# Performance work log

Measured on AMD Instinct MI355X. Metric: run time of the kernel, lower is better.

## Reference

```python
import jax, jax.numpy as jnp
import numpy as np

B, S, H = 2, 2048, 2048
NH = 16
HD = H // NH
SCALE = 1.0 / float(np.sqrt(HD))


def setup_inputs() -> dict:
    key = jax.random.key(0)
    ks = jax.random.split(key, 4)
    x = jax.random.normal(ks[0], (B, S, H), dtype=jnp.float32)
    # causal mask: 1 = attend, 0 = masked (masked_fill where mask == 0)
    attn_mask = jnp.tril(jnp.ones((S, S), dtype=jnp.int32))[None, None, :, :]
    w_qkv = jax.random.normal(ks[1], (3 * H, H), dtype=jnp.float32) * (1.0 / np.sqrt(H))
    b_qkv = jnp.zeros((3 * H,), dtype=jnp.float32)
    w_out = jax.random.normal(ks[2], (H, H), dtype=jnp.float32) * (1.0 / np.sqrt(H))
    b_out = jnp.zeros((H,), dtype=jnp.float32)
    return {"x": x, "attn_mask": attn_mask, "w_qkv": w_qkv, "b_qkv": b_qkv,
            "w_out": w_out, "b_out": b_out}


def reference(x, attn_mask, w_qkv, b_qkv, w_out, b_out):
    bsz, seq_len, hidden = x.shape
    # qkv projection (torch Linear: x @ W.T + b); TP gather is identity on 1 device
    qkv = jnp.einsum('bsh,oh->bso', x, w_qkv) + b_qkv  # [B,S,3H]
    q, k, v = jnp.split(qkv, 3, axis=-1)
    def shape(t):  # [B,S,H] -> [B,NH,S,HD]
        return t.reshape(bsz, seq_len, NH, HD).transpose(0, 2, 1, 3)
    q, k, v = shape(q), shape(k), shape(v)
    attn = jnp.einsum('bhqd,bhkd->bhqk', q, k) * SCALE  # [B,NH,S,S]
    attn = jnp.where(attn_mask == 0, jnp.float32(-10000.0), attn)
    attn = jax.nn.softmax(attn, axis=-1)  # dropout_p = 0 -> identity
    ctx = jnp.einsum('bhqk,bhkd->bhqd', attn, v)
    ctx = ctx.transpose(0, 2, 1, 3).reshape(bsz, seq_len, hidden)
    out = jnp.einsum('bsh,oh->bso', ctx, w_out) + b_out
    return out
```

## Files before the change

### kernel.cpp

```cpp
#include <hip/hip_runtime.h>
#include <hip/hip_bf16.h>
#include <stdint.h>

#define B_ 2
#define S_ 2048
#define H_ 2048
#define NH_ 16
#define HD_ 128
#define SCALE_ 0.08838834764831845f
#define QSCALE_ 0.12751743558230564f

typedef __attribute__((ext_vector_type(8))) short bf16x8;
typedef __attribute__((ext_vector_type(4))) float f32x4;

__device__ __forceinline__ unsigned short f2bf(float f) {
  union { float f; unsigned int u; } c;
  c.f = f;
  unsigned int u = c.u;
  unsigned int r = (u + 0x7fffu + ((u >> 16) & 1u)) >> 16;
  return (unsigned short)r;
}

__device__ __forceinline__ unsigned int cvt_pk_bf16(float lo, float hi) {
  unsigned int r;
  asm("v_cvt_pk_bf16_f32 %0, %1, %2" : "=v"(r) : "v"(lo), "v"(hi));
  return r;
}

__global__ void cvt_f32_bf16_k(const float* __restrict__ in,
                               unsigned short* __restrict__ out, int n4) {
  int i = blockIdx.x * blockDim.x + threadIdx.x;
  if (i < n4) {
    float4 v = reinterpret_cast<const float4*>(in)[i];
    ushort4 o;
    o.x = f2bf(v.x); o.y = f2bf(v.y); o.z = f2bf(v.z); o.w = f2bf(v.w);
    reinterpret_cast<ushort4*>(out)[i] = o;
  }
}

template <int MODE>
__global__ __launch_bounds__(256) void gemm_bt_k(
    const unsigned short* __restrict__ A,
    const unsigned short* __restrict__ Bm,
    const float* __restrict__ bias,
    int K, int N,
    float* __restrict__ outf,
    unsigned short* __restrict__ Qp,
    unsigned short* __restrict__ Kp,
    unsigned short* __restrict__ Vn) {
  __shared__ unsigned short Al[128 * 32];
  __shared__ unsigned short Bl[128 * 32];
  const int tid = threadIdx.x;
  const int lane = tid & 63;
  const int w = tid >> 6;
  const int wr = w >> 1, wc = w & 1;
  const int brow = blockIdx.y * 128, bcol = blockIdx.x * 128;
  const int lr = lane & 15, lg = lane >> 4;
  f32x4 acc[4][4] = {};

  for (int kb = 0; kb < K; kb += 32) {
    __syncthreads();
#pragma unroll
    for (int p = 0; p < 2; ++p) {
      int c = p * 256 + tid;
      int row = c >> 2, kc = (c & 3) * 8;
      __builtin_amdgcn_global_load_lds(
          (const __attribute__((address_space(1))) unsigned int*)(A + (size_t)(brow + row) * K + kb + kc),
          (__attribute__((address_space(3))) unsigned int*)(Al + c * 8), 16, 0, 0);
      __builtin_amdgcn_global_load_lds(
          (const __attribute__((address_space(1))) unsigned int*)(Bm + (size_t)(bcol + row) * K + kb + kc),
          (__attribute__((address_space(3))) unsigned int*)(Bl + c * 8), 16, 0, 0);
    }
    __syncthreads();
    bf16x8 af[4], bfr[4];
#pragma unroll
    for (int m = 0; m < 4; ++m)
      af[m] = *reinterpret_cast<const bf16x8*>(&Al[(wr * 64 + m * 16 + lr) * 32 + lg * 8]);
#pragma unroll
    for (int n = 0; n < 4; ++n)
      bfr[n] = *reinterpret_cast<const bf16x8*>(&Bl[(wc * 64 + n * 16 + lr) * 32 + lg * 8]);
#pragma unroll
    for (int m = 0; m < 4; ++m)
#pragma unroll
      for (int n = 0; n < 4; ++n)
        acc[m][n] = __builtin_amdgcn_mfma_f32_16x16x32_bf16(af[m], bfr[n], acc[m][n], 0, 0, 0);
  }

#pragma unroll
  for (int m = 0; m < 4; ++m) {
#pragma unroll
    for (int n = 0; n < 4; ++n) {
      int gcol = bcol + wc * 64 + n * 16 + lr;
      int grow0 = brow + wr * 64 + m * 16 + lg * 4;
      float bv = bias[gcol];
      if (MODE == 1) {
#pragma unroll
        for (int r = 0; r < 4; ++r)
          outf[(size_t)(grow0 + r) * N + gcol] = acc[m][n][r] + bv;
      } else {
        int region = gcol >> 11;
        int o = gcol & 2047;
        int head = o >> 7, d = o & 127;
#pragma unroll
        for (int r = 0; r < 4; ++r) {
          int grow = grow0 + r;
          int b = grow >> 11, s = grow & 2047;
          float fv = acc[m][n][r] + bv;
          if (region == 0)
            Qp[((size_t)(b * NH_ + head) * S_ + s) * HD_ + d] = f2bf(fv * QSCALE_);
          else if (region == 1)
            Kp[((size_t)(b * NH_ + head) * S_ + s) * HD_ + d] = f2bf(fv);
          else
            Vn[(size_t)grow * H_ + o] = f2bf(fv);
        }
      }
    }
  }
}

__global__ void transpose_v_k(const unsigned short* __restrict__ Vn,
                              unsigned short* __restrict__ Vt) {
  __shared__ unsigned short t[32][33];
  int bh = blockIdx.z;
  int b = bh >> 4, h = bh & 15;
  int s0 = blockIdx.x * 32, d0 = blockIdx.y * 32;
  int x = threadIdx.x, y0 = threadIdx.y;
#pragma unroll
  for (int yy = 0; yy < 32; yy += 8) {
    int s = s0 + y0 + yy;
    t[y0 + yy][x] = Vn[((size_t)(b * S_ + s)) * H_ + h * HD_ + d0 + x];
  }
  __syncthreads();
#pragma unroll
  for (int yy = 0; yy < 32; yy += 8) {
    int d = d0 + y0 + yy;
    Vt[((size_t)(bh * HD_ + d)) * S_ + s0 + x] = t[x][y0 + yy];
  }
}

__global__ __launch_bounds__(512, 4) void flash_attn_k(
    const unsigned short* __restrict__ Qp,
    const unsigned short* __restrict__ Kp,
    const unsigned short* __restrict__ Vt,
    unsigned short* __restrict__ ctx) {
  __shared__ unsigned short Kl[64 * 128];
  __shared__ unsigned short Vl[128 * 64];
  __shared__ unsigned short Pl[8][16 * 72];

  const int tid = threadIdx.x;
  const int lane = tid & 63, w = tid >> 6;
  const int lr = lane & 15, lg = lane >> 4;
  const int bid = blockIdx.x;
  const int bh = bid & 31;
  const int qi = 15 - (bid >> 5);
  const int b = bh >> 4, h = bh & 15;
  const int qtile = qi * 128;
  const int qbase = qtile + w * 16;

  const unsigned short* Qh = Qp + (size_t)bh * S_ * HD_;
  const unsigned short* Kh = Kp + (size_t)bh * S_ * HD_;
  const unsigned short* Vh = Vt + (size_t)bh * HD_ * S_;

  bf16x8 qf[4];
#pragma unroll
  for (int dc = 0; dc < 4; ++dc)
    qf[dc] = *reinterpret_cast<const bf16x8*>(Qh + (size_t)(qbase + lr) * HD_ + dc * 32 + lg * 8);

  f32x4 acc_o[8] = {};
  float m_r = -1e30f, l_r = 0.f;

  const int nkb = 2 * qi + 2;
  for (int kb = 0; kb < nkb; ++kb) {
    __syncthreads();
    const unsigned short* Kbase = Kh + (size_t)(kb * 64) * HD_;
    const unsigned short* Vbase = Vh + kb * 64;
#pragma unroll
    for (int c2 = 0; c2 < 2; ++c2) {
      int chunk = c2 * 512 + tid;
      int krow = chunk >> 4;
      int kcol = (chunk & 15) << 4;
      int kswz = kcol ^ ((krow & 7) << 4);
      __builtin_amdgcn_global_load_lds(
          (const __attribute__((address_space(1))) unsigned int*)(Kbase + krow * HD_ + (kswz >> 1)),
          (__attribute__((address_space(3))) unsigned int*)(Kl + chunk * 8), 16, 0, 0);
      int vrow = chunk >> 3;
      int vcol = (chunk & 7) << 4;
      int vswz = vcol ^ ((vrow & 7) << 4);
      __builtin_amdgcn_global_load_lds(
          (const __attribute__((address_space(1))) unsigned int*)(Vbase + (size_t)vrow * S_ + (vswz >> 1)),
          (__attribute__((address_space(3))) unsigned int*)(Vl + chunk * 8), 16, 0, 0);
    }
    __syncthreads();

    const bool live = (kb * 64 <= qbase + 15);
    if (live) {
      f32x4 sa[4] = {};
#pragma unroll
      for (int n = 0; n < 4; ++n) {
        int row = n * 16 + lr;
#pragma unroll
        for (int dc = 0; dc < 4; ++dc) {
          int byte = row * 256 + dc * 64 + lg * 16;
          byte ^= (row & 7) << 4;
          bf16x8 kf = *reinterpret_cast<const bf16x8*>(
              reinterpret_cast<const char*>(Kl) + byte);
          sa[n] = __builtin_amdgcn_mfma_f32_16x16x32_bf16(kf, qf[dc], sa[n], 0, 0, 0);
        }
      }

      if (kb * 64 + 63 > qbase) {
        int rowq = qbase + lr;
#pragma unroll
        for (int n = 0; n < 4; ++n) {
          int col0 = kb * 64 + n * 16 + lg * 4;
#pragma unroll
          for (int r = 0; r < 4; ++r)
            if (col0 + r > rowq) sa[n][r] = -1e30f;
        }
      }

      float mx4[4];
#pragma unroll
      for (int n = 0; n < 4; ++n)
        mx4[n] = fmaxf(fmaxf(sa[n][0], sa[n][1]), fmaxf(sa[n][2], sa[n][3]));
      float mx = fmaxf(fmaxf(mx4[0], mx4[1]), fmaxf(mx4[2], mx4[3]));
      mx = fmaxf(mx, __shfl_xor(mx, 16));
      mx = fmaxf(mx, __shfl_xor(mx, 32));
      float mnew = fmaxf(m_r, mx);
      float alpha = exp2f(m_r - mnew);

      float p[4][4];
      float rsn[4];
#pragma unroll
      for (int n = 0; n < 4; ++n) {
#pragma unroll
        for (int r = 0; r < 4; ++r)
          p[n][r] = exp2f(sa[n][r] - mnew);
        rsn[n] = (p[n][0] + p[n][1]) + (p[n][2] + p[n][3]);
      }
      float rs = (rsn[0] + rsn[1]) + (rsn[2] + rsn[3]);
      rs += __shfl_xor(rs, 16);
      rs += __shfl_xor(rs, 32);
      l_r = l_r * alpha + rs;
      m_r = mnew;

#pragma unroll
      for (int n = 0; n < 4; ++n) {
        uint2 pk;
        pk.x = cvt_pk_bf16(p[n][0], p[n][1]);
        pk.y = cvt_pk_bf16(p[n][2], p[n][3]);
        *reinterpret_cast<uint2*>(&Pl[w][lr * 72 + n * 16 + lg * 4]) = pk;
      }

      float al[4];
#pragma unroll
      for (int r = 0; r < 4; ++r)
        al[r] = __shfl(alpha, lg * 4 + r);
#pragma unroll
      for (int nc = 0; nc < 8; ++nc)
#pragma unroll
        for (int r = 0; r < 4; ++r)
          acc_o[nc][r] *= al[r];

      bf16x8 pa[2];
#pragma unroll
      for (int ks = 0; ks < 2; ++ks)
        pa[ks] = *reinterpret_cast<const bf16x8*>(&Pl[w][lr * 72 + ks * 32 + lg * 8]);
#pragma unroll
      for (int nc = 0; nc < 8; ++nc) {
        int row = nc * 16 + lr;
#pragma unroll
        for (int ks = 0; ks < 2; ++ks) {
          int byte = row * 128 + ks * 64 + lg * 16;
          byte ^= (row & 7) << 4;
          bf16x8 vf = *reinterpret_cast<const bf16x8*>(
              reinterpret_cast<const char*>(Vl) + byte);
          acc_o[nc] = __builtin_amdgcn_mfma_f32_16x16x32_bf16(pa[ks], vf, acc_o[nc], 0, 0, 0);
        }
      }
    }
  }

  float linv = 1.f / l_r;
  float li[4];
#pragma unroll
  for (int r = 0; r < 4; ++r)
    li[r] = __shfl(linv, lg * 4 + r);
#pragma unroll
  for (int nc = 0; nc < 8; ++nc) {
#pragma unroll
    for (int r = 0; r < 4; ++r) {
      int s = qbase + lg * 4 + r;
      ctx[((size_t)(b * S_ + s)) * H_ + h * HD_ + nc * 16 + lr] = f2bf(acc_o[nc][r] * li[r]);
    }
  }
}

extern "C" void kernel_launch(void* const* d_in, const int* in_sizes, int n_in,
                              void* d_out, int out_size, void* d_ws, size_t ws_size,
                              hipStream_t stream) {
  const float* x = (const float*)d_in[0];
  const float* w_qkv = (const float*)d_in[2];
  const float* b_qkv = (const float*)d_in[3];
  const float* w_out = (const float*)d_in[4];
  const float* b_out = (const float*)d_in[5];
  float* out = (float*)d_out;

  char* ws = (char*)d_ws;
  unsigned short* xb    = (unsigned short*)(ws);
  unsigned short* wqkvb = (unsigned short*)(ws + 16777216);
  unsigned short* woutb = (unsigned short*)(ws + 41943040);
  unsigned short* Qp    = (unsigned short*)(ws + 50331648);
  unsigned short* Kp    = (unsigned short*)(ws + 67108864);
  unsigned short* Vn    = (unsigned short*)(ws + 83886080);
  unsigned short* Vt    = (unsigned short*)(ws + 100663296);
  unsigned short* ctx   = (unsigned short*)(ws + 117440512);

  hipLaunchKernelGGL(cvt_f32_bf16_k, dim3(8192), dim3(256), 0, stream, x, xb, 2097152);
  hipLaunchKernelGGL(cvt_f32_bf16_k, dim3(12288), dim3(256), 0, stream, w_qkv, wqkvb, 3145728);
  hipLaunchKernelGGL(cvt_f32_bf16_k, dim3(4096), dim3(256), 0, stream, w_out, woutb, 1048576);

  hipLaunchKernelGGL((gemm_bt_k<0>), dim3(48, 32), dim3(256), 0, stream,
                     xb, wqkvb, b_qkv, 2048, 6144, (float*)nullptr, Qp, Kp, Vn);

  hipLaunchKernelGGL(transpose_v_k, dim3(64, 4, 32), dim3(32, 8), 0, stream, Vn, Vt);

  hipLaunchKernelGGL(flash_attn_k, dim3(512), dim3(512), 0, stream, Qp, Kp, Vt, ctx);

  hipLaunchKernelGGL((gemm_bt_k<1>), dim3(16, 32), dim3(256), 0, stream,
                     ctx, woutb, b_out, 2048, 2048, out,
                     (unsigned short*)nullptr, (unsigned short*)nullptr, (unsigned short*)nullptr);
}
```

Measured before the change: 457.8 us.

## Replace GEMM with 256x256-tile, double-buffered, 8-wave ping-pong MFMA kernel

Replaces the single-buffered 128x128 GEMM used for the QKV and output projections with a 512-thread kernel. It computes 256x256 tiles and stages 64-wide K slices into a 128 KB double-buffered, XOR-swizzled LDS region using global_load_lds. The main loop interleaves async prefetch of future K slices with MFMA phases, using explicit vmcnt/lgkmcnt waits, barriers and s_setprio. This is meant to hide global-load latency and raise MFMA utilisation. In exchange, the large tiles give fewer blocks (384 for QKV, 128 for the output projection), which risks load imbalance and idle CUs.

```diff
diff --git a/kernel.cpp b/kernel.cpp
--- a/kernel.cpp
+++ b/kernel.cpp
@@ -12,6 +12,9 @@
 
 typedef __attribute__((ext_vector_type(8))) short bf16x8;
 typedef __attribute__((ext_vector_type(4))) float f32x4;
+
+#define AS1 __attribute__((address_space(1)))
+#define AS3 __attribute__((address_space(3)))
 
 __device__ __forceinline__ unsigned short f2bf(float f) {
   union { float f; unsigned int u; } c;
@@ -39,7 +42,7 @@
 }
 
 template <int MODE>
-__global__ __launch_bounds__(256) void gemm_bt_k(
+__global__ __launch_bounds__(512, 2) void gemm8_k(
     const unsigned short* __restrict__ A,
     const unsigned short* __restrict__ Bm,
     const float* __restrict__ bias,
@@ -48,50 +51,135 @@
     unsigned short* __restrict__ Qp,
     unsigned short* __restrict__ Kp,
     unsigned short* __restrict__ Vn) {
-  __shared__ unsigned short Al[128 * 32];
-  __shared__ unsigned short Bl[128 * 32];
+  extern __shared__ char smem[];
   const int tid = threadIdx.x;
-  const int lane = tid & 63;
-  const int w = tid >> 6;
-  const int wr = w >> 1, wc = w & 1;
-  const int brow = blockIdx.y * 128, bcol = blockIdx.x * 128;
+  const int lane = tid & 63, w = tid >> 6;
+  const int wr = w >> 2, wc = w & 3;
   const int lr = lane & 15, lg = lane >> 4;
-  f32x4 acc[4][4] = {};
-
-  for (int kb = 0; kb < K; kb += 32) {
-    __syncthreads();
-#pragma unroll
-    for (int p = 0; p < 2; ++p) {
-      int c = p * 256 + tid;
-      int row = c >> 2, kc = (c & 3) * 8;
+  const int brow = blockIdx.y * 256, bcol = blockIdx.x * 256;
+  const int NT = K >> 6;
+
+  f32x4 acc[8][4] = {};
+
+  auto stageA = [&](int u, int kh) {
+#pragma unroll
+    for (int j = 0; j < 2; ++j) {
+      int chunk = j * 512 + tid;
+      int row = chunk >> 2;
+      int colb = (chunk & 3) << 4;
+      int scol = colb ^ ((row & 3) << 4);
       __builtin_amdgcn_global_load_lds(
-          (const __attribute__((address_space(1))) unsigned int*)(A + (size_t)(brow + row) * K + kb + kc),
-          (__attribute__((address_space(3))) unsigned int*)(Al + c * 8), 16, 0, 0);
+          (const AS1 unsigned int*)(A + (size_t)(brow + row) * K + u * 64 + kh * 32 + (scol >> 1)),
+          (AS3 unsigned int*)(smem + ((u & 1) * 2 + kh) * 16384 + chunk * 16), 16, 0, 0);
+    }
+  };
+  auto stageB = [&](int u, int kh) {
+#pragma unroll
+    for (int j = 0; j < 2; ++j) {
+      int chunk = j * 512 + tid;
+      int row = chunk >> 2;
+      int colb = (chunk & 3) << 4;
+      int scol = colb ^ ((row & 3) << 4);
       __builtin_amdgcn_global_load_lds(
-          (const __attribute__((address_space(1))) unsigned int*)(Bm + (size_t)(bcol + row) * K + kb + kc),
-          (__attribute__((address_space(3))) unsigned int*)(Bl + c * 8), 16, 0, 0);
-    }
-    __syncthreads();
-    bf16x8 af[4], bfr[4];
-#pragma unroll
-    for (int m = 0; m < 4; ++m)
-      af[m] = *reinterpret_cast<const bf16x8*>(&Al[(wr * 64 + m * 16 + lr) * 32 + lg * 8]);
-#pragma unroll
-    for (int n = 0; n < 4; ++n)
-      bfr[n] = *reinterpret_cast<const bf16x8*>(&Bl[(wc * 64 + n * 16 + lr) * 32 + lg * 8]);
-#pragma unroll
-    for (int m = 0; m < 4; ++m)
-#pragma unroll
-      for (int n = 0; n < 4; ++n)
-        acc[m][n] = __builtin_amdgcn_mfma_f32_16x16x32_bf16(af[m], bfr[n], acc[m][n], 0, 0, 0);
-  }
-
-#pragma unroll
-  for (int m = 0; m < 4; ++m) {
+          (const AS1 unsigned int*)(Bm + (size_t)(bcol + row) * K + u * 64 + kh * 32 + (scol >> 1)),
+          (AS3 unsigned int*)(smem + 65536 + ((u & 1) * 2 + kh) * 16384 + chunk * 16), 16, 0, 0);
+    }
+  };
+  auto ldA = [&](int d, int kh, int m) -> bf16x8 {
+    int row = wr * 128 + m * 16 + lr;
+    int byte = (d * 2 + kh) * 16384 + row * 64 + ((lg * 16) ^ ((row & 3) << 4));
+    return *reinterpret_cast<const bf16x8*>(smem + byte);
+  };
+  auto ldB = [&](int d, int kh, int n) -> bf16x8 {
+    int row = wc * 64 + n * 16 + lr;
+    int byte = 65536 + (d * 2 + kh) * 16384 + row * 64 + ((lg * 16) ^ ((row & 3) << 4));
+    return *reinterpret_cast<const bf16x8*>(smem + byte);
+  };
+
+  stageA(0, 0); stageB(0, 0); stageA(0, 1); stageB(0, 1);
+  stageA(1, 0); stageB(1, 0); stageA(1, 1);
+  asm volatile("s_waitcnt vmcnt(6)" ::: "memory");
+  __builtin_amdgcn_s_barrier();
+
+  for (int T = 0; T < NT; ++T) {
+    const int d = T & 1;
+    bf16x8 af[8], b0, b1;
+
+#pragma unroll
+    for (int m = 0; m < 8; ++m) af[m] = ldA(d, 0, m);
+    b0 = ldB(d, 0, 0); b1 = ldB(d, 0, 1);
+    if (T + 1 < NT) stageB(T + 1, 1);
+    __builtin_amdgcn_sched_barrier(0);
+    __builtin_amdgcn_s_barrier();
+    asm volatile("s_waitcnt lgkmcnt(0)" ::: "memory");
+    __builtin_amdgcn_sched_barrier(0);
+    __builtin_amdgcn_s_setprio(1);
+#pragma unroll
+    for (int m = 0; m < 8; ++m) {
+      acc[m][0] = __builtin_amdgcn_mfma_f32_16x16x32_bf16(af[m], b0, acc[m][0], 0, 0, 0);
+      acc[m][1] = __builtin_amdgcn_mfma_f32_16x16x32_bf16(af[m], b1, acc[m][1], 0, 0, 0);
+    }
+    __builtin_amdgcn_s_setprio(0);
+    __builtin_amdgcn_s_barrier();
+
+    b0 = ldB(d, 0, 2); b1 = ldB(d, 0, 3);
+    if (T + 2 < NT) stageA(T + 2, 0);
+    __builtin_amdgcn_sched_barrier(0);
+    __builtin_amdgcn_s_barrier();
+    asm volatile("s_waitcnt lgkmcnt(0)" ::: "memory");
+    __builtin_amdgcn_sched_barrier(0);
+    __builtin_amdgcn_s_setprio(1);
+#pragma unroll
+    for (int m = 0; m < 8; ++m) {
+      acc[m][2] = __builtin_amdgcn_mfma_f32_16x16x32_bf16(af[m], b0, acc[m][2], 0, 0, 0);
+      acc[m][3] = __builtin_amdgcn_mfma_f32_16x16x32_bf16(af[m], b1, acc[m][3], 0, 0, 0);
+    }
+    __builtin_amdgcn_s_setprio(0);
+    __builtin_amdgcn_s_barrier();
+
+#pragma unroll
+    for (int m = 0; m < 8; ++m) af[m] = ldA(d, 1, m);
+    b0 = ldB(d, 1, 0); b1 = ldB(d, 1, 1);
+    if (T + 2 < NT) stageB(T + 2, 0);
+    __builtin_amdgcn_sched_barrier(0);
+    __builtin_amdgcn_s_barrier();
+    asm volatile("s_waitcnt lgkmcnt(0)" ::: "memory");
+    __builtin_amdgcn_sched_barrier(0);
+    __builtin_amdgcn_s_setprio(1);
+#pragma unroll
+    for (int m = 0; m < 8; ++m) {
+      acc[m][0] = __builtin_amdgcn_mfma_f32_16x16x32_bf16(af[m], b0, acc[m][0], 0, 0, 0);
+      acc[m][1] = __builtin_amdgcn_mfma_f32_16x16x32_bf16(af[m], b1, acc[m][1], 0, 0, 0);
+    }
+    __builtin_amdgcn_s_setprio(0);
+    __builtin_amdgcn_s_barrier();
+
+    b0 = ldB(d, 1, 2); b1 = ldB(d, 1, 3);
+    if (T + 2 < NT) stageA(T + 2, 1);
+    __builtin_amdgcn_sched_barrier(0);
+    __builtin_amdgcn_s_barrier();
+    asm volatile("s_waitcnt lgkmcnt(0)" ::: "memory");
+    __builtin_amdgcn_sched_barrier(0);
+    __builtin_amdgcn_s_setprio(1);
+#pragma unroll
+    for (int m = 0; m < 8; ++m) {
+      acc[m][2] = __builtin_amdgcn_mfma_f32_16x16x32_bf16(af[m], b0, acc[m][2], 0, 0, 0);
+      acc[m][3] = __builtin_amdgcn_mfma_f32_16x16x32_bf16(af[m], b1, acc[m][3], 0, 0, 0);
+    }
+    __builtin_amdgcn_s_setprio(0);
+    if (T + 2 < NT)
+      asm volatile("s_waitcnt vmcnt(6)" ::: "memory");
+    else if (T + 1 < NT)
+      asm volatile("s_waitcnt vmcnt(0)" ::: "memory");
+    __builtin_amdgcn_s_barrier();
+  }
+
+#pragma unroll
+  for (int m = 0; m < 8; ++m) {
 #pragma unroll
     for (int n = 0; n < 4; ++n) {
       int gcol = bcol + wc * 64 + n * 16 + lr;
-      int grow0 = brow + wr * 64 + m * 16 + lg * 4;
+      int grow0 = brow + wr * 128 + m * 16 + lg * 4;
       float bv = bias[gcol];
       if (MODE == 1) {
 #pragma unroll
@@ -100,16 +188,16 @@
       } else {
         int region = gcol >> 11;
         int o = gcol & 2047;
-        int head = o >> 7, d = o & 127;
+        int head = o >> 7, dd = o & 127;
 #pragma unroll
         for (int r = 0; r < 4; ++r) {
           int grow = grow0 + r;
           int b = grow >> 11, s = grow & 2047;
           float fv = acc[m][n][r] + bv;
           if (region == 0)
-            Qp[((size_t)(b * NH_ + head) * S_ + s) * HD_ + d] = f2bf(fv * QSCALE_);
+            Qp[((size_t)(b * NH_ + head) * S_ + s) * HD_ + dd] = f2bf(fv * QSCALE_);
           else if (region == 1)
-            Kp[((size_t)(b * NH_ + head) * S_ + s) * HD_ + d] = f2bf(fv);
+            Kp[((size_t)(b * NH_ + head) * S_ + s) * HD_ + dd] = f2bf(fv);
           else
             Vn[(size_t)grow * H_ + o] = f2bf(fv);
         }
@@ -181,14 +269,14 @@
       int kcol = (chunk & 15) << 4;
       int kswz = kcol ^ ((krow & 7) << 4);
       __builtin_amdgcn_global_load_lds(
-          (const __attribute__((address_space(1))) unsigned int*)(Kbase + krow * HD_ + (kswz >> 1)),
-          (__attribute__((address_space(3))) unsigned int*)(Kl + chunk * 8), 16, 0, 0);
+          (const AS1 unsigned int*)(Kbase + krow * HD_ + (kswz >> 1)),
+          (AS3 unsigned int*)(Kl + chunk * 8), 16, 0, 0);
       int vrow = chunk >> 3;
       int vcol = (chunk & 7) << 4;
       int vswz = vcol ^ ((vrow & 7) << 4);
       __builtin_amdgcn_global_load_lds(
-          (const __attribute__((address_space(1))) unsigned int*)(Vbase + (size_t)vrow * S_ + (vswz >> 1)),
-          (__attribute__((address_space(3))) unsigned int*)(Vl + chunk * 8), 16, 0, 0);
+          (const AS1 unsigned int*)(Vbase + (size_t)vrow * S_ + (vswz >> 1)),
+          (AS3 unsigned int*)(Vl + chunk * 8), 16, 0, 0);
     }
     __syncthreads();
 
@@ -316,18 +404,23 @@
   unsigned short* Vt    = (unsigned short*)(ws + 100663296);
   unsigned short* ctx   = (unsigned short*)(ws + 117440512);
 
+  hipFuncSetAttribute(reinterpret_cast<const void*>(gemm8_k<0>),
+                      hipFuncAttributeMaxDynamicSharedMemorySize, 131072);
+  hipFuncSetAttribute(reinterpret_cast<const void*>(gemm8_k<1>),
+                      hipFuncAttributeMaxDynamicSharedMemorySize, 131072);
+
   hipLaunchKernelGGL(cvt_f32_bf16_k, dim3(8192), dim3(256), 0, stream, x, xb, 2097152);
   hipLaunchKernelGGL(cvt_f32_bf16_k, dim3(12288), dim3(256), 0, stream, w_qkv, wqkvb, 3145728);
   hipLaunchKernelGGL(cvt_f32_bf16_k, dim3(4096), dim3(256), 0, stream, w_out, woutb, 1048576);
 
-  hipLaunchKernelGGL((gemm_bt_k<0>), dim3(48, 32), dim3(256), 0, stream,
+  hipLaunchKernelGGL((gemm8_k<0>), dim3(24, 16), dim3(512), 131072, stream,
                      xb, wqkvb, b_qkv, 2048, 6144, (float*)nullptr, Qp, Kp, Vn);
 
   hipLaunchKernelGGL(transpose_v_k, dim3(64, 4, 32), dim3(32, 8), 0, stream, Vn, Vt);
 
   hipLaunchKernelGGL(flash_attn_k, dim3(512), dim3(512), 0, stream, Qp, Kp, Vt, ctx);
 
-  hipLaunchKernelGGL((gemm_bt_k<1>), dim3(16, 32), dim3(256), 0, stream,
+  hipLaunchKernelGGL((gemm8_k<1>), dim3(8, 16), dim3(512), 131072, stream,
                      ctx, woutb, b_out, 2048, 2048, out,
                      (unsigned short*)nullptr, (unsigned short*)nullptr, (unsigned short*)nullptr);
 }
```

Measured after the change: 468.7 us. 2.4% more time.

## Replace QKV projection GEMM with 256x256 double-buffered pipelined MFMA kernel

Applied to the files above, without the earlier changes.

Swaps the QKV projection GEMM for a new kernel using 256x256 block tiles, 512 threads, 64-wide K steps and double-buffered LDS (128 KB dynamic shared memory) with swizzled layout. Loads for the next K tile are interleaved between MFMA phases, with barriers and priority hints around them. The larger tile increases data reuse and hides global load latency. The cost is heavy LDS use and register pressure, and only 384 blocks on the device, which lowers occupancy. The output projection stays on the old 128x128 kernel.

```diff
diff --git a/kernel.cpp b/kernel.cpp
--- a/kernel.cpp
+++ b/kernel.cpp
@@ -7,11 +7,13 @@
 #define H_ 2048
 #define NH_ 16
 #define HD_ 128
-#define SCALE_ 0.08838834764831845f
 #define QSCALE_ 0.12751743558230564f
 
 typedef __attribute__((ext_vector_type(8))) short bf16x8;
 typedef __attribute__((ext_vector_type(4))) float f32x4;
+
+#define AS1 __attribute__((address_space(1)))
+#define AS3 __attribute__((address_space(3)))
 
 __device__ __forceinline__ unsigned short f2bf(float f) {
   union { float f; unsigned int u; } c;
@@ -38,16 +40,169 @@
   }
 }
 
-template <int MODE>
-__global__ __launch_bounds__(256) void gemm_bt_k(
+__global__ __launch_bounds__(512, 2) void gemm256_k(
     const unsigned short* __restrict__ A,
     const unsigned short* __restrict__ Bm,
     const float* __restrict__ bias,
     int K, int N,
-    float* __restrict__ outf,
     unsigned short* __restrict__ Qp,
     unsigned short* __restrict__ Kp,
     unsigned short* __restrict__ Vn) {
+  extern __shared__ char smem[];
+  const int tid = threadIdx.x;
+  const int lane = tid & 63, w = tid >> 6;
+  const int wr = w >> 2, wc = w & 3;
+  const int lr = lane & 15, lg = lane >> 4;
+  const int brow = blockIdx.y * 256, bcol = blockIdx.x * 256;
+  const int NT = K >> 6;
+
+  f32x4 acc[8][4] = {};
+
+  auto stage = [&](const unsigned short* __restrict__ src, int ldsbase,
+                   int gr0, int kc0) {
+#pragma unroll
+    for (int j = 0; j < 2; ++j) {
+      int chunk = j * 512 + tid;
+      int row = chunk >> 3;
+      int colb = (chunk & 7) << 4;
+      int scol = colb ^ (((row >> 2) & 1) << 5);
+      __builtin_amdgcn_global_load_lds(
+          (const AS1 unsigned int*)(src + (size_t)(gr0 + row) * K + kc0 + (scol >> 1)),
+          (AS3 unsigned int*)(smem + ldsbase + chunk * 16), 16, 0, 0);
+    }
+  };
+  auto aoff = [&](int d, int h) { return (d * 2 + h) * 16384; };
+  auto boff = [&](int d, int h) { return 65536 + (d * 2 + h) * 16384; };
+
+  auto ldA = [&](int d, int m, int kk) -> bf16x8 {
+    int rowr = m * 16 + lr;
+    int off = (kk * 64 + lg * 16) ^ (((rowr >> 2) & 1) << 5);
+    return *reinterpret_cast<const bf16x8*>(smem + aoff(d, wr) + rowr * 128 + off);
+  };
+  auto ldB = [&](int d, int n, int kk) -> bf16x8 {
+    int row = wc * 64 + n * 16 + lr;
+    int h = row >> 7, rowr = row & 127;
+    int off = (kk * 64 + lg * 16) ^ (((rowr >> 2) & 1) << 5);
+    return *reinterpret_cast<const bf16x8*>(smem + boff(d, h) + rowr * 128 + off);
+  };
+
+  stage(A,  aoff(0, 0), brow +   0, 0);
+  stage(A,  aoff(0, 1), brow + 128, 0);
+  stage(Bm, boff(0, 0), bcol +   0, 0);
+  stage(Bm, boff(0, 1), bcol + 128, 0);
+  stage(Bm, boff(1, 0), bcol +   0, 64);
+  stage(Bm, boff(1, 1), bcol + 128, 64);
+  asm volatile("s_waitcnt vmcnt(4)" ::: "memory");
+  __builtin_amdgcn_s_barrier();
+
+  for (int T = 0; T < NT; ++T) {
+    const int d = T & 1;
+    bf16x8 af[4][2], bA[2][2], bB[2][2];
+
+#pragma unroll
+    for (int m = 0; m < 4; ++m) { af[m][0] = ldA(d, m, 0); af[m][1] = ldA(d, m, 1); }
+    bA[0][0] = ldB(d, 0, 0); bA[0][1] = ldB(d, 0, 1);
+    bA[1][0] = ldB(d, 1, 0); bA[1][1] = ldB(d, 1, 1);
+    if (T + 1 < NT) stage(A, aoff(d ^ 1, 0), brow + 0, (T + 1) * 64);
+    __builtin_amdgcn_s_barrier();
+    asm volatile("s_waitcnt lgkmcnt(0)" ::: "memory");
+    __builtin_amdgcn_sched_barrier(0);
+    __builtin_amdgcn_s_setprio(1);
+#pragma unroll
+    for (int m = 0; m < 4; ++m)
+#pragma unroll
+      for (int n = 0; n < 2; ++n) {
+        acc[m][n] = __builtin_amdgcn_mfma_f32_16x16x32_bf16(af[m][0], bA[n][0], acc[m][n], 0, 0, 0);
+        acc[m][n] = __builtin_amdgcn_mfma_f32_16x16x32_bf16(af[m][1], bA[n][1], acc[m][n], 0, 0, 0);
+      }
+    __builtin_amdgcn_s_setprio(0);
+    __builtin_amdgcn_s_barrier();
+
+    bB[0][0] = ldB(d, 2, 0); bB[0][1] = ldB(d, 2, 1);
+    bB[1][0] = ldB(d, 3, 0); bB[1][1] = ldB(d, 3, 1);
+    if (T + 1 < NT) stage(A, aoff(d ^ 1, 1), brow + 128, (T + 1) * 64);
+    __builtin_amdgcn_s_barrier();
+    asm volatile("s_waitcnt lgkmcnt(0)" ::: "memory");
+    __builtin_amdgcn_sched_barrier(0);
+    __builtin_amdgcn_s_setprio(1);
+#pragma unroll
+    for (int m = 0; m < 4; ++m)
+#pragma unroll
+      for (int n = 0; n < 2; ++n) {
+        acc[m][n + 2] = __builtin_amdgcn_mfma_f32_16x16x32_bf16(af[m][0], bB[n][0], acc[m][n + 2], 0, 0, 0);
+        acc[m][n + 2] = __builtin_amdgcn_mfma_f32_16x16x32_bf16(af[m][1], bB[n][1], acc[m][n + 2], 0, 0, 0);
+      }
+    __builtin_amdgcn_s_setprio(0);
+    __builtin_amdgcn_s_barrier();
+
+#pragma unroll
+    for (int m = 0; m < 4; ++m) { af[m][0] = ldA(d, m + 4, 0); af[m][1] = ldA(d, m + 4, 1); }
+    if (T + 2 < NT) stage(Bm, boff(d, 0), bcol + 0, (T + 2) * 64);
+    __builtin_amdgcn_s_barrier();
+    asm volatile("s_waitcnt lgkmcnt(0)" ::: "memory");
+    __builtin_amdgcn_sched_barrier(0);
+    __builtin_amdgcn_s_setprio(1);
+#pragma unroll
+    for (int m = 0; m < 4; ++m)
+#pragma unroll
+      for (int n = 0; n < 2; ++n) {
+        acc[m + 4][n] = __builtin_amdgcn_mfma_f32_16x16x32_bf16(af[m][0], bA[n][0], acc[m + 4][n], 0, 0, 0);
+        acc[m + 4][n] = __builtin_amdgcn_mfma_f32_16x16x32_bf16(af[m][1], bA[n][1], acc[m + 4][n], 0, 0, 0);
+      }
+    __builtin_amdgcn_s_setprio(0);
+    __builtin_amdgcn_s_barrier();
+
+    if (T + 2 < NT) stage(Bm, boff(d, 1), bcol + 128, (T + 2) * 64);
+    __builtin_amdgcn_s_setprio(1);
+#pragma unroll
+    for (int m = 0; m < 4; ++m)
+#pragma unroll
+      for (int n = 0; n < 2; ++n) {
+        acc[m + 4][n + 2] = __builtin_amdgcn_mfma_f32_16x16x32_bf16(af[m][0], bB[n][0], acc[m + 4][n + 2], 0, 0, 0);
+        acc[m + 4][n + 2] = __builtin_amdgcn_mfma_f32_16x16x32_bf16(af[m][1], bB[n][1], acc[m + 4][n + 2], 0, 0, 0);
+      }
+    __builtin_amdgcn_s_setprio(0);
+    if (T + 1 < NT) {
+      if (T + 2 < NT)
+        asm volatile("s_waitcnt vmcnt(4)" ::: "memory");
+      else
+        asm volatile("s_waitcnt vmcnt(0)" ::: "memory");
+    }
+    __builtin_amdgcn_s_barrier();
+  }
+
+#pragma unroll
+  for (int m = 0; m < 8; ++m) {
+#pragma unroll
+    for (int n = 0; n < 4; ++n) {
+      int gcol = bcol + wc * 64 + n * 16 + lr;
+      int grow0 = brow + wr * 128 + m * 16 + lg * 4;
+      float bv = bias[gcol];
+      int region = gcol >> 11;
+      int o = gcol & 2047;
+      int head = o >> 7, dd = o & 127;
+#pragma unroll
+      for (int r = 0; r < 4; ++r) {
+        int grow = grow0 + r;
+        int b = grow >> 11, s = grow & 2047;
+        float fv = acc[m][n][r] + bv;
+        if (region == 0)
+          Qp[((size_t)(b * NH_ + head) * S_ + s) * HD_ + dd] = f2bf(fv * QSCALE_);
+        else if (region == 1)
+          Kp[((size_t)(b * NH_ + head) * S_ + s) * HD_ + dd] = f2bf(fv);
+        else
+          Vn[(size_t)grow * H_ + o] = f2bf(fv);
+      }
+    }
+  }
+}
+
+__global__ __launch_bounds__(256) void gemm128_k(
+    const unsigned short* __restrict__ A,
+    const unsigned short* __restrict__ Bm,
+    const float* __restrict__ bias,
+    int K, int N,
+    float* __restrict__ outf) {
   __shared__ unsigned short Al[128 * 32];
   __shared__ unsigned short Bl[128 * 32];
   const int tid = threadIdx.x;
@@ -65,11 +220,11 @@
       int c = p * 256 + tid;
       int row = c >> 2, kc = (c & 3) * 8;
       __builtin_amdgcn_global_load_lds(
-          (const __attribute__((address_space(1))) unsigned int*)(A + (size_t)(brow + row) * K + kb + kc),
-          (__attribute__((address_space(3))) unsigned int*)(Al + c * 8), 16, 0, 0);
+          (const AS1 unsigned int*)(A + (size_t)(brow + row) * K + kb + kc),
+          (AS3 unsigned int*)(Al + c * 8), 16, 0, 0);
       __builtin_amdgcn_global_load_lds(
-          (const __attribute__((address_space(1))) unsigned int*)(Bm + (size_t)(bcol + row) * K + kb + kc),
-          (__attribute__((address_space(3))) unsigned int*)(Bl + c * 8), 16, 0, 0);
+          (const AS1 unsigned int*)(Bm + (size_t)(bcol + row) * K + kb + kc),
+          (AS3 unsigned int*)(Bl + c * 8), 16, 0, 0);
     }
     __syncthreads();
     bf16x8 af[4], bfr[4];
@@ -93,27 +248,9 @@
       int gcol = bcol + wc * 64 + n * 16 + lr;
       int grow0 = brow + wr * 64 + m * 16 + lg * 4;
       float bv = bias[gcol];
-      if (MODE == 1) {
-#pragma unroll
-        for (int r = 0; r < 4; ++r)
-          outf[(size_t)(grow0 + r) * N + gcol] = acc[m][n][r] + bv;
-      } else {
-        int region = gcol >> 11;
-        int o = gcol & 2047;
-        int head = o >> 7, d = o & 127;
-#pragma unroll
-        for (int r = 0; r < 4; ++r) {
-          int grow = grow0 + r;
-          int b = grow >> 11, s = grow & 2047;
-          float fv = acc[m][n][r] + bv;
-          if (region == 0)
-            Qp[((size_t)(b * NH_ + head) * S_ + s) * HD_ + d] = f2bf(fv * QSCALE_);
-          else if (region == 1)
-            Kp[((size_t)(b * NH_ + head) * S_ + s) * HD_ + d] = f2bf(fv);
-          else
-            Vn[(size_t)grow * H_ + o] = f2bf(fv);
-        }
-      }
+#pragma unroll
+      for (int r = 0; r < 4; ++r)
+        outf[(size_t)(grow0 + r) * N + gcol] = acc[m][n][r] + bv;
     }
   }
 }
@@ -181,14 +318,14 @@
       int kcol = (chunk & 15) << 4;
       int kswz = kcol ^ ((krow & 7) << 4);
       __builtin_amdgcn_global_load_lds(
-          (const __attribute__((address_space(1))) unsigned int*)(Kbase + krow * HD_ + (kswz >> 1)),
-          (__attribute__((address_space(3))) unsigned int*)(Kl + chunk * 8), 16, 0, 0);
+          (const AS1 unsigned int*)(Kbase + krow * HD_ + (kswz >> 1)),
+          (AS3 unsigned int*)(Kl + chunk * 8), 16, 0, 0);
       int vrow = chunk >> 3;
       int vcol = (chunk & 7) << 4;
       int vswz = vcol ^ ((vrow & 7) << 4);
       __builtin_amdgcn_global_load_lds(
-          (const __attribute__((address_space(1))) unsigned int*)(Vbase + (size_t)vrow * S_ + (vswz >> 1)),
-          (__attribute__((address_space(3))) unsigned int*)(Vl + chunk * 8), 16, 0, 0);
+          (const AS1 unsigned int*)(Vbase + (size_t)vrow * S_ + (vswz >> 1)),
+          (AS3 unsigned int*)(Vl + chunk * 8), 16, 0, 0);
     }
     __syncthreads();
 
@@ -316,18 +453,20 @@
   unsigned short* Vt    = (unsigned short*)(ws + 100663296);
   unsigned short* ctx   = (unsigned short*)(ws + 117440512);
 
+  hipFuncSetAttribute(reinterpret_cast<const void*>(gemm256_k),
+                      hipFuncAttributeMaxDynamicSharedMemorySize, 131072);
+
   hipLaunchKernelGGL(cvt_f32_bf16_k, dim3(8192), dim3(256), 0, stream, x, xb, 2097152);
   hipLaunchKernelGGL(cvt_f32_bf16_k, dim3(12288), dim3(256), 0, stream, w_qkv, wqkvb, 3145728);
   hipLaunchKernelGGL(cvt_f32_bf16_k, dim3(4096), dim3(256), 0, stream, w_out, woutb, 1048576);
 
-  hipLaunchKernelGGL((gemm_bt_k<0>), dim3(48, 32), dim3(256), 0, stream,
-                     xb, wqkvb, b_qkv, 2048, 6144, (float*)nullptr, Qp, Kp, Vn);
+  hipLaunchKernelGGL(gemm256_k, dim3(24, 16), dim3(512), 131072, stream,
+                     xb, wqkvb, b_qkv, 2048, 6144, Qp, Kp, Vn);
 
   hipLaunchKernelGGL(transpose_v_k, dim3(64, 4, 32), dim3(32, 8), 0, stream, Vn, Vt);
 
   hipLaunchKernelGGL(flash_attn_k, dim3(512), dim3(512), 0, stream, Qp, Kp, Vt, ctx);
 
-  hipLaunchKernelGGL((gemm_bt_k<1>), dim3(16, 32), dim3(256), 0, stream,
-                     ctx, woutb, b_out, 2048, 2048, out,
-                     (unsigned short*)nullptr, (unsigned short*)nullptr, (unsigned short*)nullptr);
-}
+  hipLaunchKernelGGL(gemm128_k, dim3(16, 32), dim3(256), 0, stream,
+                     ctx, woutb, b_out, 2048, 2048, out);
+}
```

New measurement: 458.9 us. Within noise of the previous version (+0.2%).
